# Kernel optimization log

Measured on AMD Instinct MI355X. Metric: run time of the kernel, lower is better.

Reference implementation:

```python
import jax, jax.numpy as jnp
import numpy as np

B, S, D_IN = 32, 128, 17
D_PT, D_PAIR, D_OUT = 64, 128, 64
EPS = 1e-5


def _gelu(x):
    return jax.nn.gelu(x, approximate=False)  # torch nn.GELU default (erf)


def _bn(h, g, b):
    # BatchNorm1d (training mode): stats over batch and pair dims, per channel
    mean = h.mean(axis=(0, 1))
    var = h.var(axis=(0, 1))  # biased, matching torch normalization
    return (h - mean) * jax.lax.rsqrt(var + EPS) * g + b


def setup_inputs() -> dict:
    key = jax.random.key(0)
    ks = jax.random.split(key, 8)
    s = lambda k, shp, fan: jax.random.normal(k, shp, jnp.float32) * (1.0 / np.sqrt(fan))
    return {
        "x": jax.random.normal(ks[0], (B, S, D_IN), jnp.float32),
        # pointwise MLP: 17 -> 64 -> 64
        "w1": s(ks[1], (D_IN, D_PT), D_IN), "b1": jnp.zeros((D_PT,), jnp.float32),
        "w2": s(ks[2], (D_PT, D_PT), D_PT), "b2": jnp.zeros((D_PT,), jnp.float32),
        # pair MLP: 128 -> 128 -> 128 (input = 2 * D_PT)
        "wp1": s(ks[3], (2 * D_PT, D_PAIR), 2 * D_PT), "bp1": jnp.zeros((D_PAIR,), jnp.float32),
        "wp2": s(ks[4], (D_PAIR, D_PAIR), D_PAIR), "bp2": jnp.zeros((D_PAIR,), jnp.float32),
        # embed: BN(128) -> Conv1d(128,64,1) -> BN(64) -> GELU -> Conv1d(64,64,1) -> BN(64)
        "g0": jnp.ones((D_PAIR,), jnp.float32), "be0": jnp.zeros((D_PAIR,), jnp.float32),
        "wc1": s(ks[5], (D_PAIR, D_OUT), D_PAIR), "bc1": jnp.zeros((D_OUT,), jnp.float32),
        "g1": jnp.ones((D_OUT,), jnp.float32), "be1": jnp.zeros((D_OUT,), jnp.float32),
        "wc2": s(ks[6], (D_OUT, D_OUT), D_OUT), "bc2": jnp.zeros((D_OUT,), jnp.float32),
        "g2": jnp.ones((D_OUT,), jnp.float32), "be2": jnp.zeros((D_OUT,), jnp.float32),
    }


def reference(x, w1, b1, w2, b2, wp1, bp1, wp2, bp2,
              g0, be0, wc1, bc1, g1, be1, wc2, bc2, g2, be2):
    seq_len = x.shape[1]
    # pointwise MLP
    h = _gelu(x @ w1 + b1)
    h = _gelu(h @ w2 + b2)  # [B, S, D_PT]
    # tril pair gather (xi = features of particle j, xj = of particle i,
    # matching x_rep[b, a, c] = x[b, c] semantics in the torch code)
    i_idx, j_idx = jnp.tril_indices(seq_len)
    xi = h[:, j_idx, :]  # [B, P, D_PT]
    xj = h[:, i_idx, :]
    xij = jnp.concatenate([xi, xj], axis=-1)  # [B, P, 2*D_PT]
    # pair MLP
    e = _gelu(xij @ wp1 + bp1)
    e = _gelu(e @ wp2 + bp2)  # [B, P, D_PAIR]
    # embed stack (Conv1d k=1 == channel-wise linear)
    e = _bn(e, g0, be0)
    e = _gelu(_bn(e @ wc1 + bc1, g1, be1))
    e = _bn(e @ wc2 + bc2, g2, be2)  # [B, P, D_OUT]
    # symmetric scatter into dense pairwise output
    y = jnp.zeros((x.shape[0], seq_len, seq_len, e.shape[-1]), e.dtype)
    y = y.at[:, i_idx, j_idx, :].set(e)
    y = y.at[:, j_idx, i_idx, :].set(e)
    return y
```

## Files before the change

### kernel.cpp

```cpp
#include <hip/hip_runtime.h>
#include <hip/hip_bf16.h>
#include <math.h>

#define BB 32
#define SS 128
#define DIN 17
#define DPT 64
#define DPA 128
#define DOU 64
#define NP 8256
#define NROWS (BB * NP)
#define NCHUNK (NROWS / 128)
#define EPSF 1e-5f

typedef __hip_bfloat16 bf16;
typedef __attribute__((ext_vector_type(8))) short short8;
typedef __attribute__((ext_vector_type(16))) float f32x16;
typedef __attribute__((ext_vector_type(4))) float f32x4;
typedef __attribute__((ext_vector_type(4))) int int4v;
typedef __attribute__((ext_vector_type(4))) unsigned int uint4v;

#define MFMA32(a, b, c) __builtin_amdgcn_mfma_f32_32x32x16_bf16(a, b, c, 0, 0, 0)

__device__ __forceinline__ float bf2f(short u) {
    return __builtin_bit_cast(float, ((unsigned int)(unsigned short)u) << 16);
}

__device__ __forceinline__ void plswap(unsigned int& a, unsigned int& b) {
    asm("v_permlane32_swap_b32 %0, %1" : "+v"(a), "+v"(b));
}
__device__ __forceinline__ unsigned int cvtpk(float lo, float hi) {
    unsigned int r;
    asm("v_cvt_pk_bf16_f32 %0, %1, %2" : "=v"(r) : "v"(lo), "v"(hi));
    return r;
}

__device__ __forceinline__ void xform(const f32x16& a, short8& o0, short8& o1) {
    unsigned int w[8];
#pragma unroll
    for (int j = 0; j < 8; ++j) w[j] = cvtpk(a[2 * j], a[2 * j + 1]);
    plswap(w[0], w[2]);
    plswap(w[1], w[3]);
    plswap(w[4], w[6]);
    plswap(w[5], w[7]);
    uint4v u0 = {w[0], w[1], w[2], w[3]};
    uint4v u1 = {w[4], w[5], w[6], w[7]};
    o0 = __builtin_bit_cast(short8, u0);
    o1 = __builtin_bit_cast(short8, u1);
}

__device__ __forceinline__ float gelu_exact(float x) {
    float x2 = x * x;
    float m = fmaf(0.0356774081f, x2, 0.7978845608f);
    float e = __expf(2.0f * x * m);
    float r = __builtin_amdgcn_rcpf(e + 1.0f);
    return fmaf(-x, r, x);
}
__device__ __forceinline__ void gelu16(f32x16& a) {
#pragma unroll
    for (int r = 0; r < 16; ++r) a[r] = gelu_exact(a[r]);
}

__global__ void k_pairs(int* __restrict__ pairIJ) {
    int p = blockIdx.x * blockDim.x + threadIdx.x;
    if (p >= NP) return;
    int i = (int)((sqrtf(8.0f * (float)p + 1.0f) - 1.0f) * 0.5f);
    while ((i * (i + 1)) / 2 > p) --i;
    while (((i + 1) * (i + 2)) / 2 <= p) ++i;
    int j = p - (i * (i + 1)) / 2;
    pairIJ[p] = (i << 8) | j;
}

__global__ void k_pack(const float* __restrict__ wp1, const float* __restrict__ wp2,
                       const float* __restrict__ wc2, bf16* __restrict__ fragP1,
                       bf16* __restrict__ fragP2, bf16* __restrict__ fragC2) {
    int id = blockIdx.x * 256 + threadIdx.x;
    if (id < 16384) {
        int f = id >> 9, lane = (id >> 3) & 63, i = id & 7;
        int mt = f >> 3, s = f & 7;
        int k = s * 16 + (lane >> 5) * 8 + i;
        int m = mt * 32 + (lane & 31);
        fragP1[id] = __float2bfloat16(wp1[k * DPA + m]);
    } else if (id < 32768) {
        int rem = id - 16384;
        int f = rem >> 9, lane = (rem >> 3) & 63, i = rem & 7;
        int mt = f >> 3, s = f & 7;
        int k = s * 16 + (lane >> 5) * 8 + i;
        int m = mt * 32 + (lane & 31);
        fragP2[rem] = __float2bfloat16(wp2[k * DPA + m]);
    } else if (id < 36864) {
        int rem = id - 32768;
        int f = rem >> 9, lane = (rem >> 3) & 63, i = rem & 7;
        int mt = f >> 2, s = f & 3;
        int k = s * 16 + (lane >> 5) * 8 + i;
        int m = mt * 32 + (lane & 31);
        fragC2[rem] = __float2bfloat16(wc2[k * DOU + m]);
    }
}

__global__ void k_fold(const float* __restrict__ a0, const float* __restrict__ d0,
                       const float* __restrict__ wc1, const float* __restrict__ bc1,
                       bf16* __restrict__ fragC1, float* __restrict__ bc1p) {
    int id = blockIdx.x * 256 + threadIdx.x;
    if (id < 8192) {
        int f = id >> 9, lane = (id >> 3) & 63, i = id & 7;
        int mt = f >> 3, s = f & 7;
        int k = s * 16 + (lane >> 5) * 8 + i;
        int m = mt * 32 + (lane & 31);
        fragC1[id] = __float2bfloat16(a0[k] * wc1[k * DOU + m]);
    } else if (id < 8192 + 64) {
        int c = id - 8192;
        float s = bc1[c];
        for (int k = 0; k < DPA; ++k) s = fmaf(d0[k], wc1[k * DOU + c], s);
        bc1p[c] = s;
    }
}

__global__ void k_h(const float* __restrict__ x, const float* __restrict__ w1,
                    const float* __restrict__ b1, const float* __restrict__ w2,
                    const float* __restrict__ b2, bf16* __restrict__ h) {
    __shared__ float h1[4][DPT];
    int t = threadIdx.x;
    int rs = t >> 6;
    int c = t & 63;
    int r = blockIdx.x * 4 + rs;
    const float* xr = x + (size_t)r * DIN;
    float acc = b1[c];
#pragma unroll
    for (int k = 0; k < DIN; ++k) acc += xr[k] * w1[k * DPT + c];
    h1[rs][c] = gelu_exact(acc);
    __syncthreads();
    float acc2 = b2[c];
#pragma unroll
    for (int k = 0; k < DPT; ++k) acc2 += h1[rs][k] * w2[k * DPT + c];
    h[(size_t)r * DPT + c] = __float2bfloat16(gelu_exact(acc2));
}

__global__ __launch_bounds__(256, 3) void k_e0m(
    const bf16* __restrict__ h, const int* __restrict__ pairIJ,
    const short8* __restrict__ fragP1, const short8* __restrict__ fragP2,
    const float* __restrict__ bp1, const float* __restrict__ bp2,
    bf16* __restrict__ e0, float* __restrict__ part) {
    __shared__ __align__(16) char lds[49152];
    int t = threadIdx.x;
    int w = t >> 6, l = t & 63;
    int l31 = l & 31, lhi = l >> 5;
    int row0 = blockIdx.x * 128;
    int prow = w * 32 + l31;

    for (int u = t; u < 3072; u += 256) {
        short8 v = (u < 1024) ? fragP1[1024 + u] : fragP2[u - 1024];
        *(short8*)(lds + u * 16) = v;
    }

    short8 Wa[16];
#pragma unroll
    for (int i = 0; i < 16; ++i) Wa[i] = fragP1[i * 64 + l];

    int n = row0 + prow;
    int b = n / NP, p = n - b * NP;
    int ij = pairIJ[p];
    const bf16* hj = h + (((size_t)(b * SS + (ij & 255))) << 6);
    const bf16* hi = h + (((size_t)(b * SS + (ij >> 8))) << 6);
    short8 bx[8];
#pragma unroll
    for (int s = 0; s < 4; ++s) {
        bx[s] = *(const short8*)(hj + s * 16 + lhi * 8);
        bx[s + 4] = *(const short8*)(hi + s * 16 + lhi * 8);
    }
    __syncthreads();

    short8 B2[8];
    {
        f32x16 c0, c1;
#pragma unroll
        for (int g = 0; g < 4; ++g) {
            f32x4 v0 = *(const f32x4*)(bp1 + 0 * 32 + g * 8 + lhi * 4);
            f32x4 v1 = *(const f32x4*)(bp1 + 1 * 32 + g * 8 + lhi * 4);
#pragma unroll
            for (int j = 0; j < 4; ++j) { c0[g * 4 + j] = v0[j]; c1[g * 4 + j] = v1[j]; }
        }
#pragma unroll
        for (int s = 0; s < 8; ++s) {
            c0 = MFMA32(Wa[s], bx[s], c0);
            c1 = MFMA32(Wa[8 + s], bx[s], c1);
        }
        gelu16(c0);
        xform(c0, B2[0], B2[1]);
        gelu16(c1);
        xform(c1, B2[2], B2[3]);
    }
    {
        f32x16 c2, c3;
#pragma unroll
        for (int g = 0; g < 4; ++g) {
            f32x4 v0 = *(const f32x4*)(bp1 + 2 * 32 + g * 8 + lhi * 4);
            f32x4 v1 = *(const f32x4*)(bp1 + 3 * 32 + g * 8 + lhi * 4);
#pragma unroll
            for (int j = 0; j < 4; ++j) { c2[g * 4 + j] = v0[j]; c3[g * 4 + j] = v1[j]; }
        }
#pragma unroll
        for (int s = 0; s < 8; ++s) {
            short8 a2 = *(const short8*)(lds + (s * 64 + l) * 16);
            short8 a3 = *(const short8*)(lds + ((8 + s) * 64 + l) * 16);
            c2 = MFMA32(a2, bx[s], c2);
            c3 = MFMA32(a3, bx[s], c3);
        }
        gelu16(c2);
        xform(c2, B2[4], B2[5]);
        gelu16(c3);
        xform(c3, B2[6], B2[7]);
    }

    short8 o[8];
#pragma unroll
    for (int mp = 0; mp < 2; ++mp) {
        f32x16 c0, c1;
#pragma unroll
        for (int g = 0; g < 4; ++g) {
            f32x4 v0 = *(const f32x4*)(bp2 + (2 * mp) * 32 + g * 8 + lhi * 4);
            f32x4 v1 = *(const f32x4*)(bp2 + (2 * mp + 1) * 32 + g * 8 + lhi * 4);
#pragma unroll
            for (int j = 0; j < 4; ++j) { c0[g * 4 + j] = v0[j]; c1[g * 4 + j] = v1[j]; }
        }
#pragma unroll
        for (int s = 0; s < 8; ++s) {
            short8 a0 = *(const short8*)(lds + 16384 + (((2 * mp) * 8 + s) * 64 + l) * 16);
            short8 a1 = *(const short8*)(lds + 16384 + (((2 * mp + 1) * 8 + s) * 64 + l) * 16);
            c0 = MFMA32(a0, B2[s], c0);
            c1 = MFMA32(a1, B2[s], c1);
        }
        gelu16(c0);
        xform(c0, o[4 * mp + 0], o[4 * mp + 1]);
        gelu16(c1);
        xform(c1, o[4 * mp + 2], o[4 * mp + 3]);
    }
    __syncthreads();

    char* stg = lds + 16384 + w * 8192;
#pragma unroll
    for (int mt = 0; mt < 4; ++mt) {
        int slot0 = 4 * mt + lhi, slot1 = 4 * mt + 2 + lhi;
        *(short8*)(stg + l31 * 256 + ((slot0 * 16) ^ ((l31 & 15) << 4))) = o[2 * mt];
        *(short8*)(stg + l31 * 256 + ((slot1 * 16) ^ ((l31 & 15) << 4))) = o[2 * mt + 1];
    }

    float sum[8], sq[8];
#pragma unroll
    for (int i = 0; i < 8; ++i) { sum[i] = 0.f; sq[i] = 0.f; }
    int slot = l & 15;
#pragma unroll
    for (int q = 0; q < 8; ++q) {
        int r = (l >> 4) + 4 * q;
        short8 v = *(const short8*)(stg + r * 256 + ((slot * 16) ^ ((r & 15) << 4)));
        *(short8*)(e0 + (size_t)(row0 + w * 32 + r) * DPA + slot * 8) = v;
#pragma unroll
        for (int i = 0; i < 8; ++i) {
            float f = bf2f(v[i]);
            sum[i] += f;
            sq[i] += f * f;
        }
    }

    float* sb = (float*)stg;
#pragma unroll
    for (int i = 0; i < 8; ++i) {
        sb[l * 17 + i] = sum[i];
        sb[l * 17 + 8 + i] = sq[i];
    }
    __syncthreads();

    {
        int c = t & 127, isq = t >> 7;
        float s = 0.f;
#pragma unroll
        for (int wv = 0; wv < 4; ++wv) {
            const float* sv = (const float*)(lds + 16384 + wv * 8192);
#pragma unroll
            for (int g = 0; g < 4; ++g)
                s += sv[(g * 16 + (c >> 3)) * 17 + isq * 8 + (c & 7)];
        }
        part[(size_t)blockIdx.x * 256 + t] = s;
    }
}

__global__ void k_stats(const float* __restrict__ part, int nch, int nblk,
                        float* __restrict__ a, float* __restrict__ d,
                        const float* __restrict__ g, const float* __restrict__ be) {
    int c = blockIdx.x;
    __shared__ float ssum[256], ssq[256];
    float s = 0.f, q = 0.f;
    for (int bidx = threadIdx.x; bidx < nblk; bidx += 256) {
        s += part[(size_t)bidx * (2 * nch) + c];
        q += part[(size_t)bidx * (2 * nch) + nch + c];
    }
    ssum[threadIdx.x] = s;
    ssq[threadIdx.x] = q;
    __syncthreads();
    for (int w = 128; w > 0; w >>= 1) {
        if ((int)threadIdx.x < w) {
            ssum[threadIdx.x] += ssum[threadIdx.x + w];
            ssq[threadIdx.x] += ssq[threadIdx.x + w];
        }
        __syncthreads();
    }
    if (threadIdx.x == 0) {
        float mean = ssum[0] / (float)NROWS;
        float var = ssq[0] / (float)NROWS - mean * mean;
        float rstd = rsqrtf(var + EPSF);
        float aa = g[c] * rstd;
        a[c] = aa;
        d[c] = be[c] - mean * aa;
    }
}

__global__ __launch_bounds__(256) void k_e1m(
    const bf16* __restrict__ e0, const short8* __restrict__ fragC1,
    const float* __restrict__ bc1p, bf16* __restrict__ e1,
    float* __restrict__ part) {
    __shared__ __align__(16) char buf[16384];
    int t = threadIdx.x;
    int w = t >> 6, l = t & 63;
    int l31 = l & 31, lhi = l >> 5;
    int row0 = blockIdx.x * 128;
    int prow = w * 32 + l31;

    short8 Wc[16];
#pragma unroll
    for (int i = 0; i < 16; ++i) Wc[i] = fragC1[i * 64 + l];
    short8 B[8];
#pragma unroll
    for (int s = 0; s < 8; ++s)
        B[s] = *(const short8*)(e0 + (size_t)(row0 + prow) * DPA + s * 16 + lhi * 8);

    f32x16 acc[2];
#pragma unroll
    for (int mt = 0; mt < 2; ++mt)
#pragma unroll
        for (int g = 0; g < 4; ++g) {
            f32x4 bv = *(const f32x4*)(bc1p + mt * 32 + g * 8 + lhi * 4);
#pragma unroll
            for (int j = 0; j < 4; ++j) acc[mt][g * 4 + j] = bv[j];
        }
#pragma unroll
    for (int s = 0; s < 8; ++s) {
        acc[0] = MFMA32(Wc[s], B[s], acc[0]);
        acc[1] = MFMA32(Wc[8 + s], B[s], acc[1]);
    }

#pragma unroll
    for (int mt = 0; mt < 2; ++mt) {
        short8 o0, o1;
        xform(acc[mt], o0, o1);
        int slot0 = 4 * mt + lhi, slot1 = 4 * mt + 2 + lhi;
        *(short8*)(buf + prow * 128 + ((slot0 * 16) ^ ((prow & 7) << 4))) = o0;
        *(short8*)(buf + prow * 128 + ((slot1 * 16) ^ ((prow & 7) << 4))) = o1;
    }
    __syncthreads();

    float sum[8], sq[8];
#pragma unroll
    for (int i = 0; i < 8; ++i) { sum[i] = 0.f; sq[i] = 0.f; }
    int slot = t & 7;
#pragma unroll
    for (int q = 0; q < 4; ++q) {
        int rr = (t >> 3) + 32 * q;
        short8 v = *(const short8*)(buf + rr * 128 + ((slot * 16) ^ ((rr & 7) << 4)));
        *(short8*)(e1 + (size_t)(row0 + rr) * DOU + slot * 8) = v;
#pragma unroll
        for (int i = 0; i < 8; ++i) {
            float f = bf2f(v[i]);
            sum[i] += f;
            sq[i] += f * f;
        }
    }
    __syncthreads();
    float* bb = (float*)buf;
#pragma unroll
    for (int i = 0; i < 8; ++i) {
        bb[t * 16 + i] = sum[i];
        bb[t * 16 + 8 + i] = sq[i];
    }
    __syncthreads();
    if (t < 128) {
        int c = t & 63, isq = t >> 6;
        float s = 0.f;
#pragma unroll
        for (int g = 0; g < 32; ++g)
            s += bb[((c >> 3) + 8 * g) * 16 + isq * 8 + (c & 7)];
        part[(size_t)blockIdx.x * 128 + t] = s;
    }
}

__global__ __launch_bounds__(256) void k_e2m(
    const bf16* __restrict__ e1, const float* __restrict__ a1,
    const float* __restrict__ d1, const short8* __restrict__ fragC2,
    const float* __restrict__ bc2, bf16* __restrict__ e2,
    float* __restrict__ part) {
    __shared__ __align__(16) char buf[16384];
    int t = threadIdx.x;
    int w = t >> 6, l = t & 63;
    int l31 = l & 31, lhi = l >> 5;
    int row0 = blockIdx.x * 128;
    int prow = w * 32 + l31;

    short8 Wc[8];
#pragma unroll
    for (int s = 0; s < 8; ++s) Wc[s] = fragC2[s * 64 + l];

    short8 B[4];
#pragma unroll
    for (int s = 0; s < 4; ++s) {
        short8 raw = *(const short8*)(e1 + (size_t)(row0 + prow) * DOU + s * 16 + lhi * 8);
        int c0 = s * 16 + lhi * 8;
        f32x4 av0 = *(const f32x4*)(a1 + c0), av1 = *(const f32x4*)(a1 + c0 + 4);
        f32x4 dv0 = *(const f32x4*)(d1 + c0), dv1 = *(const f32x4*)(d1 + c0 + 4);
        float gg[8];
#pragma unroll
        for (int i = 0; i < 4; ++i) gg[i] = gelu_exact(fmaf(bf2f(raw[i]), av0[i], dv0[i]));
#pragma unroll
        for (int i = 0; i < 4; ++i) gg[4 + i] = gelu_exact(fmaf(bf2f(raw[4 + i]), av1[i], dv1[i]));
        uint4v u = {cvtpk(gg[0], gg[1]), cvtpk(gg[2], gg[3]),
                    cvtpk(gg[4], gg[5]), cvtpk(gg[6], gg[7])};
        B[s] = __builtin_bit_cast(short8, u);
    }

    f32x16 acc[2];
#pragma unroll
    for (int mt = 0; mt < 2; ++mt)
#pragma unroll
        for (int g = 0; g < 4; ++g) {
            f32x4 bv = *(const f32x4*)(bc2 + mt * 32 + g * 8 + lhi * 4);
#pragma unroll
            for (int j = 0; j < 4; ++j) acc[mt][g * 4 + j] = bv[j];
        }
#pragma unroll
    for (int s = 0; s < 4; ++s) {
        acc[0] = MFMA32(Wc[s], B[s], acc[0]);
        acc[1] = MFMA32(Wc[4 + s], B[s], acc[1]);
    }

#pragma unroll
    for (int mt = 0; mt < 2; ++mt) {
        short8 o0, o1;
        xform(acc[mt], o0, o1);
        int slot0 = 4 * mt + lhi, slot1 = 4 * mt + 2 + lhi;
        *(short8*)(buf + prow * 128 + ((slot0 * 16) ^ ((prow & 7) << 4))) = o0;
        *(short8*)(buf + prow * 128 + ((slot1 * 16) ^ ((prow & 7) << 4))) = o1;
    }
    __syncthreads();

    float sum[8], sq[8];
#pragma unroll
    for (int i = 0; i < 8; ++i) { sum[i] = 0.f; sq[i] = 0.f; }
    int slot = t & 7;
#pragma unroll
    for (int q = 0; q < 4; ++q) {
        int rr = (t >> 3) + 32 * q;
        short8 v = *(const short8*)(buf + rr * 128 + ((slot * 16) ^ ((rr & 7) << 4)));
        *(short8*)(e2 + (size_t)(row0 + rr) * DOU + slot * 8) = v;
#pragma unroll
        for (int i = 0; i < 8; ++i) {
            float f = bf2f(v[i]);
            sum[i] += f;
            sq[i] += f * f;
        }
    }
    __syncthreads();
    float* bb = (float*)buf;
#pragma unroll
    for (int i = 0; i < 8; ++i) {
        bb[t * 16 + i] = sum[i];
        bb[t * 16 + 8 + i] = sq[i];
    }
    __syncthreads();
    if (t < 128) {
        int c = t & 63, isq = t >> 6;
        float s = 0.f;
#pragma unroll
        for (int g = 0; g < 32; ++g)
            s += bb[((c >> 3) + 8 * g) * 16 + isq * 8 + (c & 7)];
        part[(size_t)blockIdx.x * 128 + t] = s;
    }
}

__global__ void k_out(const bf16* __restrict__ e2, const int* __restrict__ pairIJ,
                      const float* __restrict__ a2, const float* __restrict__ d2,
                      float* __restrict__ y) {
    int t = threadIdx.x;
    int n = blockIdx.x * 32 + (t >> 3);
    int c0 = (t & 7) * 8;
    int b = n / NP, p = n - b * NP;
    int ij = pairIJ[p];
    int ii = ij >> 8, jj = ij & 255;
    short8 raw = *(const short8*)(e2 + (size_t)n * DOU + c0);
    f32x4 aLo = *(const f32x4*)(a2 + c0), aHi = *(const f32x4*)(a2 + c0 + 4);
    f32x4 dLo = *(const f32x4*)(d2 + c0), dHi = *(const f32x4*)(d2 + c0 + 4);
    f32x4 v0, v1;
#pragma unroll
    for (int i = 0; i < 4; ++i) v0[i] = fmaf(bf2f(raw[i]), aLo[i], dLo[i]);
#pragma unroll
    for (int i = 0; i < 4; ++i) v1[i] = fmaf(bf2f(raw[4 + i]), aHi[i], dHi[i]);
    float* y1 = y + ((size_t)(b * SS + ii) * SS + jj) * DOU + c0;
    float* y2 = y + ((size_t)(b * SS + jj) * SS + ii) * DOU + c0;
    *(f32x4*)y1 = v0;
    *(f32x4*)(y1 + 4) = v1;
    *(f32x4*)y2 = v0;
    *(f32x4*)(y2 + 4) = v1;
}

extern "C" void kernel_launch(void* const* d_in, const int* in_sizes, int n_in,
                              void* d_out, int out_size, void* d_ws, size_t ws_size,
                              hipStream_t stream) {
    const float* x   = (const float*)d_in[0];
    const float* w1  = (const float*)d_in[1];
    const float* b1  = (const float*)d_in[2];
    const float* w2  = (const float*)d_in[3];
    const float* b2  = (const float*)d_in[4];
    const float* wp1 = (const float*)d_in[5];
    const float* bp1 = (const float*)d_in[6];
    const float* wp2 = (const float*)d_in[7];
    const float* bp2 = (const float*)d_in[8];
    const float* g0  = (const float*)d_in[9];
    const float* be0 = (const float*)d_in[10];
    const float* wc1 = (const float*)d_in[11];
    const float* bc1 = (const float*)d_in[12];
    const float* g1  = (const float*)d_in[13];
    const float* be1 = (const float*)d_in[14];
    const float* wc2 = (const float*)d_in[15];
    const float* bc2 = (const float*)d_in[16];
    const float* g2  = (const float*)d_in[17];
    const float* be2 = (const float*)d_in[18];

    char* ws = (char*)d_ws;
    const size_t OFF_PAIR   = 0;
    const size_t OFF_H      = 33280;
    const size_t OFF_PART   = 557568;
    const size_t OFF_FRAGP1 = 2671104;
    const size_t OFF_FRAGP2 = 2703872;
    const size_t OFF_FRAGC1 = 2736640;
    const size_t OFF_FRAGC2 = 2753024;
    const size_t OFF_BC1P   = 2761216;
    const size_t OFF_A0 = 2761472, OFF_D0 = 2761984;
    const size_t OFF_A1 = 2762496, OFF_D1 = 2762752;
    const size_t OFF_A2 = 2763008, OFF_D2 = 2763264;
    const size_t OFF_E2 = 2763520;

    int*   pairIJ = (int*)(ws + OFF_PAIR);
    bf16*  h      = (bf16*)(ws + OFF_H);
    float* part   = (float*)(ws + OFF_PART);
    bf16*  fragP1 = (bf16*)(ws + OFF_FRAGP1);
    bf16*  fragP2 = (bf16*)(ws + OFF_FRAGP2);
    bf16*  fragC1 = (bf16*)(ws + OFF_FRAGC1);
    bf16*  fragC2 = (bf16*)(ws + OFF_FRAGC2);
    float* bc1p   = (float*)(ws + OFF_BC1P);
    float* a0 = (float*)(ws + OFF_A0);
    float* d0 = (float*)(ws + OFF_D0);
    float* a1 = (float*)(ws + OFF_A1);
    float* d1 = (float*)(ws + OFF_D1);
    float* a2 = (float*)(ws + OFF_A2);
    float* d2 = (float*)(ws + OFF_D2);
    bf16*  e2 = (bf16*)(ws + OFF_E2);

    bf16* e0 = (bf16*)d_out;
    bf16* e1 = (bf16*)((char*)d_out + (size_t)NROWS * DPA * sizeof(bf16));
    float* y = (float*)d_out;

    k_pairs<<<(NP + 255) / 256, 256, 0, stream>>>(pairIJ);
    k_pack<<<144, 256, 0, stream>>>(wp1, wp2, wc2, fragP1, fragP2, fragC2);
    k_h<<<(BB * SS) / 4, 256, 0, stream>>>(x, w1, b1, w2, b2, h);
    k_e0m<<<NCHUNK, 256, 0, stream>>>(h, pairIJ, (const short8*)fragP1,
                                      (const short8*)fragP2, bp1, bp2, e0, part);
    k_stats<<<DPA, 256, 0, stream>>>(part, DPA, NCHUNK, a0, d0, g0, be0);
    k_fold<<<33, 256, 0, stream>>>(a0, d0, wc1, bc1, fragC1, bc1p);
    k_e1m<<<NCHUNK, 256, 0, stream>>>(e0, (const short8*)fragC1, bc1p, e1, part);
    k_stats<<<DOU, 256, 0, stream>>>(part, DOU, NCHUNK, a1, d1, g1, be1);
    k_e2m<<<NCHUNK, 256, 0, stream>>>(e1, a1, d1, (const short8*)fragC2, bc2, e2, part);
    k_stats<<<DOU, 256, 0, stream>>>(part, DOU, NCHUNK, a2, d2, g2, be2);
    k_out<<<NROWS / 32, 256, 0, stream>>>(e2, pairIJ, a2, d2, y);
}
```

Measured before the change: 158.7 us.

## Factor first pair-MLP layer into per-particle projections summed per pair

The first pair layer acts on concat(h_j, h_i), so it is split into u = h·Wp1_top + bp1 and v = h·Wp1_bot, computed once per particle in k_h. The pair kernel then forms gelu(u_j + v_i) elementwise instead of running the 128x128 MFMA layer for every pair. This cuts the first-layer matmul work by about a factor of S and shrinks the weight staging in LDS. The cost is that k_h now streams wp1 through shared memory in every block, gathered u/v rows are twice as wide as h, and u/v are rounded to bf16 before the add.

Measured after the change: 173.5 us. 1.09x slower.

```diff
diff --git a/kernel.cpp b/kernel.cpp
--- a/kernel.cpp
+++ b/kernel.cpp
@@ -17,7 +17,6 @@
 typedef __attribute__((ext_vector_type(8))) short short8;
 typedef __attribute__((ext_vector_type(16))) float f32x16;
 typedef __attribute__((ext_vector_type(4))) float f32x4;
-typedef __attribute__((ext_vector_type(4))) int int4v;
 typedef __attribute__((ext_vector_type(4))) unsigned int uint4v;
 
 #define MFMA32(a, b, c) __builtin_amdgcn_mfma_f32_32x32x16_bf16(a, b, c, 0, 0, 0)
@@ -71,8 +70,7 @@
     pairIJ[p] = (i << 8) | j;
 }
 
-__global__ void k_pack(const float* __restrict__ wp1, const float* __restrict__ wp2,
-                       const float* __restrict__ wc2, bf16* __restrict__ fragP1,
+__global__ void k_pack(const float* __restrict__ wp2, const float* __restrict__ wc2,
                        bf16* __restrict__ fragP2, bf16* __restrict__ fragC2) {
     int id = blockIdx.x * 256 + threadIdx.x;
     if (id < 16384) {
@@ -80,16 +78,9 @@
         int mt = f >> 3, s = f & 7;
         int k = s * 16 + (lane >> 5) * 8 + i;
         int m = mt * 32 + (lane & 31);
-        fragP1[id] = __float2bfloat16(wp1[k * DPA + m]);
-    } else if (id < 32768) {
+        fragP2[id] = __float2bfloat16(wp2[k * DPA + m]);
+    } else if (id < 20480) {
         int rem = id - 16384;
-        int f = rem >> 9, lane = (rem >> 3) & 63, i = rem & 7;
-        int mt = f >> 3, s = f & 7;
-        int k = s * 16 + (lane >> 5) * 8 + i;
-        int m = mt * 32 + (lane & 31);
-        fragP2[rem] = __float2bfloat16(wp2[k * DPA + m]);
-    } else if (id < 36864) {
-        int rem = id - 32768;
         int f = rem >> 9, lane = (rem >> 3) & 63, i = rem & 7;
         int mt = f >> 2, s = f & 3;
         int k = s * 16 + (lane >> 5) * 8 + i;
@@ -116,13 +107,16 @@
     }
 }
 
-__global__ void k_h(const float* __restrict__ x, const float* __restrict__ w1,
-                    const float* __restrict__ b1, const float* __restrict__ w2,
-                    const float* __restrict__ b2, bf16* __restrict__ h) {
+__global__ __launch_bounds__(256) void k_h(
+    const float* __restrict__ x, const float* __restrict__ w1,
+    const float* __restrict__ b1, const float* __restrict__ w2,
+    const float* __restrict__ b2, const float* __restrict__ wp1,
+    const float* __restrict__ bp1, bf16* __restrict__ u, bf16* __restrict__ v) {
     __shared__ float h1[4][DPT];
+    __shared__ float h2[4][DPT];
+    __shared__ float wt[128][64];
     int t = threadIdx.x;
-    int rs = t >> 6;
-    int c = t & 63;
+    int rs = t >> 6, c = t & 63;
     int r = blockIdx.x * 4 + rs;
     const float* xr = x + (size_t)r * DIN;
     float acc = b1[c];
@@ -133,84 +127,61 @@
     float acc2 = b2[c];
 #pragma unroll
     for (int k = 0; k < DPT; ++k) acc2 += h1[rs][k] * w2[k * DPT + c];
-    h[(size_t)r * DPT + c] = __float2bfloat16(gelu_exact(acc2));
+    h2[rs][c] = gelu_exact(acc2);
+
+    for (int cp = 0; cp < 2; ++cp) {
+        __syncthreads();
+        for (int idx = t; idx < 8192; idx += 256) {
+            int k = idx >> 6, cc = idx & 63;
+            wt[k][cc] = wp1[k * DPA + cp * 64 + cc];
+        }
+        __syncthreads();
+        float au = bp1[cp * 64 + c], av = 0.f;
+#pragma unroll
+        for (int k = 0; k < 64; ++k) {
+            float hk = h2[rs][k];
+            au = fmaf(hk, wt[k][c], au);
+            av = fmaf(hk, wt[64 + k][c], av);
+        }
+        u[(size_t)r * DPA + cp * 64 + c] = __float2bfloat16(au);
+        v[(size_t)r * DPA + cp * 64 + c] = __float2bfloat16(av);
+    }
 }
 
 __global__ __launch_bounds__(256, 3) void k_e0m(
-    const bf16* __restrict__ h, const int* __restrict__ pairIJ,
-    const short8* __restrict__ fragP1, const short8* __restrict__ fragP2,
-    const float* __restrict__ bp1, const float* __restrict__ bp2,
-    bf16* __restrict__ e0, float* __restrict__ part) {
-    __shared__ __align__(16) char lds[49152];
+    const bf16* __restrict__ u, const bf16* __restrict__ v,
+    const int* __restrict__ pairIJ, const short8* __restrict__ fragP2,
+    const float* __restrict__ bp2, bf16* __restrict__ e0,
+    float* __restrict__ part) {
+    __shared__ __align__(16) char lds[32768];
     int t = threadIdx.x;
     int w = t >> 6, l = t & 63;
     int l31 = l & 31, lhi = l >> 5;
     int row0 = blockIdx.x * 128;
     int prow = w * 32 + l31;
 
-    for (int u = t; u < 3072; u += 256) {
-        short8 v = (u < 1024) ? fragP1[1024 + u] : fragP2[u - 1024];
-        *(short8*)(lds + u * 16) = v;
-    }
-
-    short8 Wa[16];
-#pragma unroll
-    for (int i = 0; i < 16; ++i) Wa[i] = fragP1[i * 64 + l];
+    for (int uq = t; uq < 2048; uq += 256)
+        *(short8*)(lds + uq * 16) = fragP2[uq];
 
     int n = row0 + prow;
     int b = n / NP, p = n - b * NP;
     int ij = pairIJ[p];
-    const bf16* hj = h + (((size_t)(b * SS + (ij & 255))) << 6);
-    const bf16* hi = h + (((size_t)(b * SS + (ij >> 8))) << 6);
-    short8 bx[8];
-#pragma unroll
-    for (int s = 0; s < 4; ++s) {
-        bx[s] = *(const short8*)(hj + s * 16 + lhi * 8);
-        bx[s + 4] = *(const short8*)(hi + s * 16 + lhi * 8);
-    }
-    __syncthreads();
-
+    const bf16* ur = u + (((size_t)(b * SS + (ij & 255))) << 7);
+    const bf16* vr = v + (((size_t)(b * SS + (ij >> 8))) << 7);
     short8 B2[8];
-    {
-        f32x16 c0, c1;
-#pragma unroll
-        for (int g = 0; g < 4; ++g) {
-            f32x4 v0 = *(const f32x4*)(bp1 + 0 * 32 + g * 8 + lhi * 4);
-            f32x4 v1 = *(const f32x4*)(bp1 + 1 * 32 + g * 8 + lhi * 4);
-#pragma unroll
-            for (int j = 0; j < 4; ++j) { c0[g * 4 + j] = v0[j]; c1[g * 4 + j] = v1[j]; }
-        }
-#pragma unroll
-        for (int s = 0; s < 8; ++s) {
-            c0 = MFMA32(Wa[s], bx[s], c0);
-            c1 = MFMA32(Wa[8 + s], bx[s], c1);
-        }
-        gelu16(c0);
-        xform(c0, B2[0], B2[1]);
-        gelu16(c1);
-        xform(c1, B2[2], B2[3]);
-    }
-    {
-        f32x16 c2, c3;
-#pragma unroll
-        for (int g = 0; g < 4; ++g) {
-            f32x4 v0 = *(const f32x4*)(bp1 + 2 * 32 + g * 8 + lhi * 4);
-            f32x4 v1 = *(const f32x4*)(bp1 + 3 * 32 + g * 8 + lhi * 4);
-#pragma unroll
-            for (int j = 0; j < 4; ++j) { c2[g * 4 + j] = v0[j]; c3[g * 4 + j] = v1[j]; }
-        }
-#pragma unroll
-        for (int s = 0; s < 8; ++s) {
-            short8 a2 = *(const short8*)(lds + (s * 64 + l) * 16);
-            short8 a3 = *(const short8*)(lds + ((8 + s) * 64 + l) * 16);
-            c2 = MFMA32(a2, bx[s], c2);
-            c3 = MFMA32(a3, bx[s], c3);
-        }
-        gelu16(c2);
-        xform(c2, B2[4], B2[5]);
-        gelu16(c3);
-        xform(c3, B2[6], B2[7]);
-    }
+#pragma unroll
+    for (int s = 0; s < 8; ++s) {
+        short8 us = *(const short8*)(ur + s * 16 + lhi * 8);
+        short8 vs = *(const short8*)(vr + s * 16 + lhi * 8);
+        float g[8];
+#pragma unroll
+        for (int i = 0; i < 8; ++i)
+            g[i] = gelu_exact(bf2f(us[i]) + bf2f(vs[i]));
+        uint4v pk = {cvtpk(g[0], g[1]), cvtpk(g[2], g[3]),
+                     cvtpk(g[4], g[5]), cvtpk(g[6], g[7])};
+        B2[s] = __builtin_bit_cast(short8, pk);
+    }
+    __syncthreads();
 
     short8 o[8];
 #pragma unroll
@@ -225,8 +196,8 @@
         }
 #pragma unroll
         for (int s = 0; s < 8; ++s) {
-            short8 a0 = *(const short8*)(lds + 16384 + (((2 * mp) * 8 + s) * 64 + l) * 16);
-            short8 a1 = *(const short8*)(lds + 16384 + (((2 * mp + 1) * 8 + s) * 64 + l) * 16);
+            short8 a0 = *(const short8*)(lds + (((2 * mp) * 8 + s) * 64 + l) * 16);
+            short8 a1 = *(const short8*)(lds + (((2 * mp + 1) * 8 + s) * 64 + l) * 16);
             c0 = MFMA32(a0, B2[s], c0);
             c1 = MFMA32(a1, B2[s], c1);
         }
@@ -237,7 +208,7 @@
     }
     __syncthreads();
 
-    char* stg = lds + 16384 + w * 8192;
+    char* stg = lds + w * 8192;
 #pragma unroll
     for (int mt = 0; mt < 4; ++mt) {
         int slot0 = 4 * mt + lhi, slot1 = 4 * mt + 2 + lhi;
@@ -252,11 +223,11 @@
 #pragma unroll
     for (int q = 0; q < 8; ++q) {
         int r = (l >> 4) + 4 * q;
-        short8 v = *(const short8*)(stg + r * 256 + ((slot * 16) ^ ((r & 15) << 4)));
-        *(short8*)(e0 + (size_t)(row0 + w * 32 + r) * DPA + slot * 8) = v;
+        short8 vv = *(const short8*)(stg + r * 256 + ((slot * 16) ^ ((r & 15) << 4)));
+        *(short8*)(e0 + (size_t)(row0 + w * 32 + r) * DPA + slot * 8) = vv;
 #pragma unroll
         for (int i = 0; i < 8; ++i) {
-            float f = bf2f(v[i]);
+            float f = bf2f(vv[i]);
             sum[i] += f;
             sq[i] += f * f;
         }
@@ -275,7 +246,7 @@
         float s = 0.f;
 #pragma unroll
         for (int wv = 0; wv < 4; ++wv) {
-            const float* sv = (const float*)(lds + 16384 + wv * 8192);
+            const float* sv = (const float*)(lds + wv * 8192);
 #pragma unroll
             for (int g = 0; g < 4; ++g)
                 s += sv[(g * 16 + (c >> 3)) * 17 + isq * 8 + (c & 7)];
@@ -420,9 +391,9 @@
         for (int i = 0; i < 4; ++i) gg[i] = gelu_exact(fmaf(bf2f(raw[i]), av0[i], dv0[i]));
 #pragma unroll
         for (int i = 0; i < 4; ++i) gg[4 + i] = gelu_exact(fmaf(bf2f(raw[4 + i]), av1[i], dv1[i]));
-        uint4v u = {cvtpk(gg[0], gg[1]), cvtpk(gg[2], gg[3]),
-                    cvtpk(gg[4], gg[5]), cvtpk(gg[6], gg[7])};
-        B[s] = __builtin_bit_cast(short8, u);
+        uint4v uu = {cvtpk(gg[0], gg[1]), cvtpk(gg[2], gg[3]),
+                     cvtpk(gg[4], gg[5]), cvtpk(gg[6], gg[7])};
+        B[s] = __builtin_bit_cast(short8, uu);
     }
 
     f32x16 acc[2];
@@ -534,9 +505,7 @@
 
     char* ws = (char*)d_ws;
     const size_t OFF_PAIR   = 0;
-    const size_t OFF_H      = 33280;
     const size_t OFF_PART   = 557568;
-    const size_t OFF_FRAGP1 = 2671104;
     const size_t OFF_FRAGP2 = 2703872;
     const size_t OFF_FRAGC1 = 2736640;
     const size_t OFF_FRAGC2 = 2753024;
@@ -547,9 +516,7 @@
     const size_t OFF_E2 = 2763520;
 
     int*   pairIJ = (int*)(ws + OFF_PAIR);
-    bf16*  h      = (bf16*)(ws + OFF_H);
     float* part   = (float*)(ws + OFF_PART);
-    bf16*  fragP1 = (bf16*)(ws + OFF_FRAGP1);
     bf16*  fragP2 = (bf16*)(ws + OFF_FRAGP2);
     bf16*  fragC1 = (bf16*)(ws + OFF_FRAGC1);
     bf16*  fragC2 = (bf16*)(ws + OFF_FRAGC2);
@@ -564,13 +531,14 @@
 
     bf16* e0 = (bf16*)d_out;
     bf16* e1 = (bf16*)((char*)d_out + (size_t)NROWS * DPA * sizeof(bf16));
+    bf16* u  = (bf16*)((char*)d_out + 101449728);
+    bf16* v  = (bf16*)((char*)d_out + 102498304);
     float* y = (float*)d_out;
 
     k_pairs<<<(NP + 255) / 256, 256, 0, stream>>>(pairIJ);
-    k_pack<<<144, 256, 0, stream>>>(wp1, wp2, wc2, fragP1, fragP2, fragC2);
-    k_h<<<(BB * SS) / 4, 256, 0, stream>>>(x, w1, b1, w2, b2, h);
-    k_e0m<<<NCHUNK, 256, 0, stream>>>(h, pairIJ, (const short8*)fragP1,
-                                      (const short8*)fragP2, bp1, bp2, e0, part);
+    k_pack<<<80, 256, 0, stream>>>(wp2, wc2, fragP2, fragC2);
+    k_h<<<(BB * SS) / 4, 256, 0, stream>>>(x, w1, b1, w2, b2, wp1, bp1, u, v);
+    k_e0m<<<NCHUNK, 256, 0, stream>>>(u, v, pairIJ, (const short8*)fragP2, bp2, e0, part);
     k_stats<<<DPA, 256, 0, stream>>>(part, DPA, NCHUNK, a0, d0, g0, be0);
     k_fold<<<33, 256, 0, stream>>>(a0, d0, wc1, bc1, fragC1, bc1p);
     k_e1m<<<NCHUNK, 256, 0, stream>>>(e0, (const short8*)fragC1, bc1p, e1, part);
```
